# Optimization experiments

Hardware: AMD Instinct MI355X
Metric: run time of the kernel (lower is better)

The kernel has to match this reference:

```python
import jax, jax.numpy as jnp
import numpy as np


def _pn_layer(x, W):
    # x: [B, d]; W: [N, d+1, d+1]. z = [x, 1]; out[b, n] = z_b^T W_n z_b
    z = jnp.concatenate([x, jnp.ones((x.shape[0], 1), dtype=x.dtype)], axis=1)  # [B, d+1]
    zW = jnp.einsum('bi,nij->bnj', z, W)      # [B, N, d+1]
    return jnp.einsum('bnj,bj->bn', zW, z)    # [B, N]


def setup_inputs() -> dict:
    key = jax.random.key(0)
    k_x, k1, k2, k3, kw, kb = jax.random.split(key, 6)
    B, D = 2048, 256
    return {
        'x': jax.random.normal(k_x, (B, D), dtype=jnp.float32),
        'W1': jax.random.normal(k1, (256, D + 1, D + 1), dtype=jnp.float32),
        'W2': jax.random.normal(k2, (256, 257, 257), dtype=jnp.float32),
        'W3': jax.random.normal(k3, (256, 257, 257), dtype=jnp.float32),
        'w_out': jax.random.normal(kw, (1, 256), dtype=jnp.float32),
        'b_out': jax.random.normal(kb, (1,), dtype=jnp.float32),
    }


def reference(x, W1, W2, W3, w_out, b_out):
    h = _pn_layer(x, W1)   # [B, 256]
    h = _pn_layer(h, W2)   # [B, 256]
    h = _pn_layer(h, W3)   # [B, 256]
    return h @ w_out.T + b_out  # [B, 1]
```

## Files before the change

### kernel.cpp

```cpp
#include <hip/hip_runtime.h>
#include <hip/hip_bf16.h>

typedef __attribute__((ext_vector_type(8))) short short8;
typedef __attribute__((ext_vector_type(4))) float f32x4;

#define DDIM 256
#define WROW 257
#define WSTRIDE 66049
#define WT3_N 36864

__device__ __forceinline__ unsigned short f2bf(float f) {
    unsigned int u = __float_as_uint(f);
    u += 0x7fff + ((u >> 16) & 1);
    return (unsigned short)(u >> 16);
}
__device__ __forceinline__ float bf2f(unsigned short s) {
    return __uint_as_float(((unsigned int)s) << 16);
}


__global__ __launch_bounds__(256) void conv_w3_kernel(
    const float* __restrict__ Wf, unsigned short* __restrict__ Wt3,
    float* __restrict__ Vt, float* __restrict__ Dv)
{
    __shared__ float tKJ[64][65];
    __shared__ float tJK[64][65];
    const int TJ[10] = {0,1,1,2,2,2,3,3,3,3};
    const int TK[10] = {0,0,1,0,1,2,0,1,2,3};
    const int tid = threadIdx.x;
    const int n   = blockIdx.y;
    const int tj  = TJ[blockIdx.x];
    const int tk  = TK[blockIdx.x];
    const float* Wn = Wf + (size_t)n * WSTRIDE;
    if (blockIdx.x == 0) {
        int j = tid;
        Vt[n * 256 + j] = Wn[(size_t)j * WROW + 256] + Wn[65792 + j];
        if (j == 0) Dv[n] = Wn[66048];
    }
    #pragma unroll
    for (int it = 0; it < 4; ++it) {
        int idx = it * 256 + tid;
        int r   = idx >> 4;
        int c4  = (idx & 15) * 4;
        float4 vKJ = *reinterpret_cast<const float4*>(&Wn[(size_t)(tk * 64 + r) * WROW + tj * 64 + c4]);
        float4 vJK = *reinterpret_cast<const float4*>(&Wn[(size_t)(tj * 64 + r) * WROW + tk * 64 + c4]);
        tKJ[r][c4 + 0] = vKJ.x; tKJ[r][c4 + 1] = vKJ.y; tKJ[r][c4 + 2] = vKJ.z; tKJ[r][c4 + 3] = vKJ.w;
        tJK[r][c4 + 0] = vJK.x; tJK[r][c4 + 1] = vJK.y; tJK[r][c4 + 2] = vJK.z; tJK[r][c4 + 3] = vJK.w;
    }
    __syncthreads();
    const int wv = tid >> 6, lane = tid & 63;
    unsigned short* out = Wt3 + (size_t)n * WT3_N;
    int ch[8]; int nch = 0;
    #pragma unroll
    for (int jtl = 0; jtl < 2; ++jtl)
        #pragma unroll
        for (int kkl = 0; kkl < 2; ++kkl) {
            if (tk * 2 + kkl <= tj * 2 + jtl) {
                ch[nch++] = jtl * 4 + kkl * 2 + 0;
                ch[nch++] = jtl * 4 + kkl * 2 + 1;
            }
        }
    for (int c = wv; c < nch; c += 4) {
        const int jtl = ch[c] >> 2, kkl = (ch[c] >> 1) & 1, half = ch[c] & 1;
        const int jtg = tj * 2 + jtl, kkg = tk * 2 + kkl;
        const float sc = (kkg == jtg) ? 0.5f : 1.0f;
        const int jl = jtl * 32 + half * 16 + (lane & 15);
        const int k0 = kkl * 32 + (lane >> 4) * 8;
        unsigned int w[4];
        #pragma unroll
        for (int t = 0; t < 4; ++t) {
            float lo = sc * (tKJ[k0 + 2 * t][jl]     + tJK[jl][k0 + 2 * t]);
            float hi = sc * (tKJ[k0 + 2 * t + 1][jl] + tJK[jl][k0 + 2 * t + 1]);
            w[t] = (unsigned)f2bf(lo) | ((unsigned)f2bf(hi) << 16);
        }
        size_t sidx = (size_t)(jtg * (jtg + 1) / 2 + kkg) * 1024 + half * 512 + lane * 8;
        *reinterpret_cast<uint4*>(out + sidx) = make_uint4(w[0], w[1], w[2], w[3]);
    }
}

__device__ __forceinline__ void xe_gather3(const unsigned short* T, unsigned short* Xe2,
                                           int bx, int tid) {
    const int lane = tid & 63, g = tid >> 6, qw = (tid >> 4) & 3, r15 = tid & 15;
    #pragma unroll
    for (int it = 0; it < 16; ++it) {
        int c  = g * 16 + it;
        int h  = c >> 5;
        int jt = (c >> 2) & 7;
        int m  = c & 3;
        int rbase = h * 64 + m * 16 + qw * 4;
        int jA = jt * 32 + r15;
        unsigned int u0 = T[(rbase + 0) * 256 + jA];
        unsigned int u1 = T[(rbase + 1) * 256 + jA];
        unsigned int u2 = T[(rbase + 2) * 256 + jA];
        unsigned int u3 = T[(rbase + 3) * 256 + jA];
        unsigned int v0 = T[(rbase + 0) * 256 + jA + 16];
        unsigned int v1 = T[(rbase + 1) * 256 + jA + 16];
        unsigned int v2 = T[(rbase + 2) * 256 + jA + 16];
        unsigned int v3 = T[(rbase + 3) * 256 + jA + 16];
        uint4 w = make_uint4(u0 | (u1 << 16), u2 | (u3 << 16),
                             v0 | (v1 << 16), v2 | (v3 << 16));
        *reinterpret_cast<uint4*>(Xe2 + ((size_t)(bx * 2 + h) * 16384 + jt * 2048 + m * 512 + lane * 8)) = w;
    }
}

__global__ __launch_bounds__(256) void conv_x_rm_kernel(
    const float* __restrict__ X, unsigned short* __restrict__ Xbf, unsigned short* __restrict__ Xe2)
{
    __shared__ __align__(16) unsigned short T[128 * 256];
    const int tid = threadIdx.x;
    const int b0 = blockIdx.x * 128;
    const float4* Xv = reinterpret_cast<const float4*>(X + (size_t)b0 * 256);
    uint2* Xo = reinterpret_cast<uint2*>(Xbf + (size_t)b0 * 256);
    #pragma unroll
    for (int it = 0; it < 32; ++it) {
        int idx4 = it * 256 + tid;
        float4 v = Xv[idx4];
        uint2 p;
        p.x = (unsigned)f2bf(v.x) | ((unsigned)f2bf(v.y) << 16);
        p.y = (unsigned)f2bf(v.z) | ((unsigned)f2bf(v.w) << 16);
        *reinterpret_cast<uint2*>(&T[idx4 * 4]) = p;
        Xo[idx4] = p;
    }
    __syncthreads();
    xe_gather3(T, Xe2, blockIdx.x, tid);
}

__global__ __launch_bounds__(256) void conv_x_tr_kernel(
    const unsigned short* __restrict__ Hsrc, unsigned short* __restrict__ Xbf,
    unsigned short* __restrict__ Xe2)
{
    __shared__ __align__(16) unsigned short T[128 * 256];
    const int tid = threadIdx.x;
    const int b0 = blockIdx.x * 128;
    #pragma unroll
    for (int it = 0; it < 64; ++it) {
        int lin = it * 256 + tid;
        int k = lin >> 6, bp = lin & 63;
        unsigned int v = *reinterpret_cast<const unsigned int*>(Hsrc + (size_t)k * 2048 + b0 + bp * 2);
        T[(bp * 2) * 256 + k]     = (unsigned short)(v & 0xffff);
        T[(bp * 2 + 1) * 256 + k] = (unsigned short)(v >> 16);
    }
    __syncthreads();
    uint4* Xo = reinterpret_cast<uint4*>(Xbf + (size_t)b0 * 256);
    #pragma unroll
    for (int it = 0; it < 16; ++it) {
        int idx8 = it * 256 + tid;
        Xo[idx8] = *reinterpret_cast<uint4*>(&T[idx8 * 8]);
    }
    xe_gather3(T, Xe2, blockIdx.x, tid);
}

__global__ __launch_bounds__(256, 3) void pn10_kernel(
    const unsigned short* __restrict__ Xbf,
    const unsigned short* __restrict__ Xe2,
    const unsigned short* __restrict__ Wt3,
    const float* __restrict__ Vt,
    const float* __restrict__ Dv,
    unsigned short* __restrict__ Ht)
{
    __shared__ __align__(16) char Xl[32768];

    const int tid  = threadIdx.x;
    const int lane = tid & 63;
    const int wv   = tid >> 6;
    const int qw   = lane >> 4;
    const int r15  = lane & 15;

    const int fid = blockIdx.y * 32 + blockIdx.x;
    const int bt  = (fid >> 3) & 31;
    const int ng  = (fid & 7) + ((fid >> 8) << 3);
    const int n   = ng * 4 + wv;
    const int b0  = bt * 64;

    {
        const uint4* xs = reinterpret_cast<const uint4*>(Xbf + (size_t)b0 * 256);
        #pragma unroll
        for (int c = 0; c < 8; ++c) {
            int idx = c * 256 + tid;
            uint4 v = xs[idx];
            int L = idx * 16;
            int d = L ^ (((L >> 9) & 7) << 4);
            *reinterpret_cast<uint4*>(&Xl[d]) = v;
        }
    }

    const unsigned short* wp = Wt3 + (size_t)n * WT3_N + (size_t)lane * 8;
    const float* vn = Vt + n * 256;
    const unsigned short* xe = Xe2 + (size_t)bt * 16384 + (size_t)lane * 8;

    short8 bA0 = *reinterpret_cast<const short8*>(wp);
    short8 bB0 = *reinterpret_cast<const short8*>(wp + 512);
    short8 bA1 = *reinterpret_cast<const short8*>(wp + 1024);
    short8 bB1 = *reinterpret_cast<const short8*>(wp + 1024 + 512);
    short8 bA2 = *reinterpret_cast<const short8*>(wp + 2048);
    short8 bB2 = *reinterpret_cast<const short8*>(wp + 2048 + 512);
    short8 bA3 = *reinterpret_cast<const short8*>(wp + 3072);
    short8 bB3 = *reinterpret_cast<const short8*>(wp + 3072 + 512);

    short8 e0 = *reinterpret_cast<const short8*>(xe);
    short8 e1 = *reinterpret_cast<const short8*>(xe + 512);
    short8 e2 = *reinterpret_cast<const short8*>(xe + 1024);
    short8 e3 = *reinterpret_cast<const short8*>(xe + 1536);
    float vA = vn[r15], vB = vn[16 + r15];

    float ps[4][4];
    f32x4 a0[4], a1[4];
    #pragma unroll
    for (int m = 0; m < 4; ++m) {
        a0[m] = f32x4{0.f, 0.f, 0.f, 0.f};
        a1[m] = f32x4{0.f, 0.f, 0.f, 0.f};
        #pragma unroll
        for (int r = 0; r < 4; ++r) ps[m][r] = 0.f;
    }

    int jt = 0, kk = 0;
    int slab_pf = 4;

    __syncthreads();

    auto body = [&](short8& bA, short8& bB) {
        #pragma unroll
        for (int m = 0; m < 4; ++m) {
            const int row = m * 16 + r15;
            const int byte = (row * 512 + kk * 64 + qw * 16) ^ ((row & 7) << 4);
            short8 a = *reinterpret_cast<const short8*>(&Xl[byte]);
            a0[m] = __builtin_amdgcn_mfma_f32_16x16x32_bf16(a, bA, a0[m], 0, 0, 0);
            a1[m] = __builtin_amdgcn_mfma_f32_16x16x32_bf16(a, bB, a1[m], 0, 0, 0);
        }
        if (kk == jt) {
            #pragma unroll
            for (int r = 0; r < 4; ++r) {
                ps[0][r] += (a0[0][r] + vA) * bf2f((unsigned short)e0[r]) + (a1[0][r] + vB) * bf2f((unsigned short)e0[4 + r]);
                ps[1][r] += (a0[1][r] + vA) * bf2f((unsigned short)e1[r]) + (a1[1][r] + vB) * bf2f((unsigned short)e1[4 + r]);
                ps[2][r] += (a0[2][r] + vA) * bf2f((unsigned short)e2[r]) + (a1[2][r] + vB) * bf2f((unsigned short)e2[4 + r]);
                ps[3][r] += (a0[3][r] + vA) * bf2f((unsigned short)e3[r]) + (a1[3][r] + vB) * bf2f((unsigned short)e3[4 + r]);
            }
            #pragma unroll
            for (int m = 0; m < 4; ++m) {
                a0[m] = f32x4{0.f, 0.f, 0.f, 0.f};
                a1[m] = f32x4{0.f, 0.f, 0.f, 0.f};
            }
            jt += 1; kk = 0;
            const int jc = (jt < 8) ? jt : 7;
            e0 = *reinterpret_cast<const short8*>(xe + jc * 2048);
            e1 = *reinterpret_cast<const short8*>(xe + jc * 2048 + 512);
            e2 = *reinterpret_cast<const short8*>(xe + jc * 2048 + 1024);
            e3 = *reinterpret_cast<const short8*>(xe + jc * 2048 + 1536);
            vA = vn[jc * 32 + r15];
            vB = vn[jc * 32 + 16 + r15];
        } else {
            kk += 1;
        }
        const int sc = (slab_pf <= 35) ? slab_pf : 35;
        const unsigned short* pf = wp + (size_t)sc * 1024;
        bA = *reinterpret_cast<const short8*>(pf);
        bB = *reinterpret_cast<const short8*>(pf + 512);
        slab_pf += 1;
    };

    #pragma unroll 1
    for (int i = 0; i < 9; ++i) {
        body(bA0, bB0);
        body(bA1, bB1);
        body(bA2, bB2);
        body(bA3, bB3);
    }

    #pragma unroll
    for (int off = 1; off <= 8; off <<= 1)
        #pragma unroll
        for (int m = 0; m < 4; ++m)
            #pragma unroll
            for (int r = 0; r < 4; ++r) ps[m][r] += __shfl_xor(ps[m][r], off, 64);

    if (r15 == 0) {
        const float dn = Dv[n];
        #pragma unroll
        for (int m = 0; m < 4; ++m)
            #pragma unroll
            for (int r = 0; r < 4; ++r)
                Ht[(size_t)n * 2048 + b0 + m * 16 + qw * 4 + r] = f2bf(ps[m][r] + dn);
    }
}

__global__ __launch_bounds__(256) void out_tr_kernel(
    const unsigned short* __restrict__ H3, const float* __restrict__ w_out,
    const float* __restrict__ b_out, float* __restrict__ out)
{
    __shared__ float red2[256];
    const int tid = threadIdx.x;
    const int b = blockIdx.x * 128 + (tid & 127);
    const int half = tid >> 7;
    float s = 0.f;
    #pragma unroll 8
    for (int k = 0; k < 128; ++k) {
        int nn = half * 128 + k;
        s += bf2f(H3[(size_t)nn * 2048 + b]) * w_out[nn];
    }
    red2[tid] = s;
    __syncthreads();
    if (tid < 128) out[b] = red2[tid] + red2[tid + 128] + b_out[0];
}


__global__ __launch_bounds__(256, 2) void pn_layer_kernel(
    const float* __restrict__ X, const float* __restrict__ W, float* __restrict__ H)
{
    __shared__ __align__(16) char Xl[64 * 256 * 2];
    __shared__ __align__(16) char Wl[2][256 * 32 * 2];
    const int tid  = threadIdx.x;
    const int lane = tid & 63;
    const int wv   = tid >> 6;
    const int qw   = lane >> 4;
    const int r15  = lane & 15;
    const int n  = blockIdx.y;
    const int b0 = blockIdx.x * 64;
    const float* Wn = W + (size_t)n * WSTRIDE;
    {
        const float4* Xv = reinterpret_cast<const float4*>(X + (size_t)b0 * DDIM);
        #pragma unroll
        for (int it = 0; it < 16; ++it) {
            int idx4 = tid + it * 256;
            int r = idx4 >> 6, c4 = idx4 & 63;
            float4 v = Xv[r * 64 + c4];
            uint2 p;
            p.x = (unsigned)f2bf(v.x) | ((unsigned)f2bf(v.y) << 16);
            p.y = (unsigned)f2bf(v.z) | ((unsigned)f2bf(v.w) << 16);
            int byte = (r * 512 + c4 * 8) ^ ((r & 7) << 4);
            *reinterpret_cast<uint2*>(&Xl[byte]) = p;
        }
    }
    f32x4 acc[4][4];
    #pragma unroll
    for (int nf = 0; nf < 4; ++nf) {
        int j = wv * 64 + nf * 16 + r15;
        float vj = Wn[(size_t)j * WROW + 256] + Wn[65792 + j];
        #pragma unroll
        for (int m = 0; m < 4; ++m) acc[m][nf] = f32x4{vj, vj, vj, vj};
    }
    auto stageW = [&](int buf, int kk) {
        const int k0 = kk * 32;
        const int j  = tid;
        float t[32];
        #pragma unroll
        for (int k = 0; k < 32; ++k) t[k] = Wn[(size_t)(k0 + k) * WROW + j];
        char* Wb = Wl[buf];
        #pragma unroll
        for (int g = 0; g < 4; ++g) {
            unsigned int p0 = (unsigned)f2bf(t[g*8+0]) | ((unsigned)f2bf(t[g*8+1]) << 16);
            unsigned int p1 = (unsigned)f2bf(t[g*8+2]) | ((unsigned)f2bf(t[g*8+3]) << 16);
            unsigned int p2 = (unsigned)f2bf(t[g*8+4]) | ((unsigned)f2bf(t[g*8+5]) << 16);
            unsigned int p3 = (unsigned)f2bf(t[g*8+6]) | ((unsigned)f2bf(t[g*8+7]) << 16);
            int byte = (j * 64 + g * 16) ^ ((j & 7) << 4);
            *reinterpret_cast<uint4*>(&Wb[byte]) = make_uint4(p0, p1, p2, p3);
        }
    };
    auto computeK = [&](int buf, int kk) {
        char* Wb = Wl[buf];
        short8 a[4], bbf[4];
        #pragma unroll
        for (int m = 0; m < 4; ++m) {
            int row = m * 16 + r15;
            int byte = (row * 512 + kk * 64 + qw * 16) ^ ((row & 7) << 4);
            a[m] = *reinterpret_cast<short8*>(&Xl[byte]);
        }
        #pragma unroll
        for (int nf = 0; nf < 4; ++nf) {
            int j = wv * 64 + nf * 16 + r15;
            int byte = (j * 64 + qw * 16) ^ ((j & 7) << 4);
            bbf[nf] = *reinterpret_cast<short8*>(&Wb[byte]);
        }
        #pragma unroll
        for (int m = 0; m < 4; ++m)
            #pragma unroll
            for (int nf = 0; nf < 4; ++nf)
                acc[m][nf] = __builtin_amdgcn_mfma_f32_16x16x32_bf16(a[m], bbf[nf], acc[m][nf], 0, 0, 0);
    };
    stageW(0, 0);
    int cur = 0;
    #pragma unroll
    for (int kk = 0; kk < 8; ++kk) {
        __syncthreads();
        if (kk < 7) stageW(cur ^ 1, kk + 1);
        computeK(cur, kk);
        cur ^= 1;
    }
    float ps[16];
    #pragma unroll
    for (int i = 0; i < 16; ++i) ps[i] = 0.f;
    #pragma unroll
    for (int m = 0; m < 4; ++m)
        #pragma unroll
        for (int nf = 0; nf < 4; ++nf) {
            int j = wv * 64 + nf * 16 + r15;
            #pragma unroll
            for (int r = 0; r < 4; ++r) {
                int brow = m * 16 + qw * 4 + r;
                int byte = (brow * 512 + j * 2) ^ ((brow & 7) << 4);
                float xv = bf2f(*reinterpret_cast<unsigned short*>(&Xl[byte]));
                ps[m * 4 + r] += acc[m][nf][r] * xv;
            }
        }
    #pragma unroll
    for (int off = 1; off <= 8; off <<= 1)
        #pragma unroll
        for (int i = 0; i < 16; ++i) ps[i] += __shfl_xor(ps[i], off, 64);
    __syncthreads();
    float* red = reinterpret_cast<float*>(Wl);
    if (r15 == 0) {
        #pragma unroll
        for (int m = 0; m < 4; ++m)
            #pragma unroll
            for (int r = 0; r < 4; ++r)
                red[wv * 64 + m * 16 + qw * 4 + r] = ps[m * 4 + r];
    }
    __syncthreads();
    if (tid < 64) {
        float s = red[tid] + red[64 + tid] + red[128 + tid] + red[192 + tid] + Wn[66048];
        H[(size_t)(b0 + tid) * DDIM + n] = s;
    }
}

__global__ __launch_bounds__(256) void out_kernel(
    const float* __restrict__ H, const float* __restrict__ w_out,
    const float* __restrict__ b_out, float* __restrict__ out)
{
    int b = blockIdx.x * 4 + (threadIdx.x >> 6);
    int lane = threadIdx.x & 63;
    const float* h = H + (size_t)b * 256;
    float s = 0.f;
    #pragma unroll
    for (int c = 0; c < 4; ++c) s += h[lane + c * 64] * w_out[lane + c * 64];
    #pragma unroll
    for (int off = 1; off < 64; off <<= 1) s += __shfl_xor(s, off, 64);
    if (lane == 0) out[b] = s + b_out[0];
}

extern "C" void kernel_launch(void* const* d_in, const int* in_sizes, int n_in,
                              void* d_out, int out_size, void* d_ws, size_t ws_size,
                              hipStream_t stream) {
    const float* x    = (const float*)d_in[0];
    const float* W1   = (const float*)d_in[1];
    const float* W2   = (const float*)d_in[2];
    const float* W3   = (const float*)d_in[3];
    const float* wout = (const float*)d_in[4];
    const float* bout = (const float*)d_in[5];
    float* out = (float*)d_out;

    const size_t WT3_BYTES = (size_t)256 * WT3_N * 2;
    const size_t XB_BYTES  = (size_t)2048 * 256 * 2;
    const size_t XE2_BYTES = (size_t)32 * 16384 * 2;
    const size_t VT_BYTES  = 256 * 256 * 4;
    const size_t DV_BYTES  = 1024;
    const size_t HT_BYTES  = (size_t)256 * 2048 * 2;
    const size_t need = WT3_BYTES + XB_BYTES + XE2_BYTES + VT_BYTES + DV_BYTES + HT_BYTES;

    dim3 blk(256, 1, 1);

    if (ws_size >= need) {
        char* p = (char*)d_ws;
        unsigned short* Wt3 = (unsigned short*)p;              p += WT3_BYTES;
        unsigned short* Xbf = (unsigned short*)p;              p += XB_BYTES;
        unsigned short* Xe2 = (unsigned short*)p;              p += XE2_BYTES;
        float*          Vt  = (float*)p;                       p += VT_BYTES;
        float*          Dv  = (float*)p;                       p += DV_BYTES;
        unsigned short* Ht  = (unsigned short*)p;

        const float* Ws[3] = {W1, W2, W3};

        dim3 wgrid(10, 256), lgrid(32, 64), xgrid(16);
        for (int L = 0; L < 3; ++L) {
            if (L == 0) conv_x_rm_kernel<<<xgrid, blk, 0, stream>>>(x, Xbf, Xe2);
            else        conv_x_tr_kernel<<<xgrid, blk, 0, stream>>>(Ht, Xbf, Xe2);
            conv_w3_kernel<<<wgrid, blk, 0, stream>>>(Ws[L], Wt3, Vt, Dv);
            pn10_kernel<<<lgrid, blk, 0, stream>>>(Xbf, Xe2, Wt3, Vt, Dv, Ht);
        }
        out_tr_kernel<<<xgrid, blk, 0, stream>>>(Ht, wout, bout, out);
    } else {
        float* h1 = (float*)d_ws;
        float* h2 = h1 + 2048 * 256;
        dim3 grid(32, 256);
        pn_layer_kernel<<<grid, blk, 0, stream>>>(x,  W1, h1);
        pn_layer_kernel<<<grid, blk, 0, stream>>>(h1, W2, h2);
        pn_layer_kernel<<<grid, blk, 0, stream>>>(h2, W3, h1);
        out_kernel<<<512, blk, 0, stream>>>(h1, wout, bout, out);
    }
}
```

Baseline: 272.7 us.

## Process two output neurons per wave to reuse X tile LDS reads

Each wave now computes two output neurons (n0, n1) instead of one, so every LDS load of the activation fragment feeds four MFMAs instead of two. The grid is halved in y and launch bounds drop to 2 blocks per CU to make room for the doubled accumulators. Prefetch depth falls from four slabs to two double-buffered slabs, and the Xe/V loads move from prefetched registers to on-demand loads at each triangle boundary. This trades lower occupancy and less latency hiding for fewer LDS reads and less X-tile staging per neuron.

```diff
diff --git a/kernel.cpp b/kernel.cpp
--- a/kernel.cpp
+++ b/kernel.cpp
@@ -150,7 +150,7 @@
     xe_gather3(T, Xe2, blockIdx.x, tid);
 }
 
-__global__ __launch_bounds__(256, 3) void pn10_kernel(
+__global__ __launch_bounds__(256, 2) void pn13_kernel(
     const unsigned short* __restrict__ Xbf,
     const unsigned short* __restrict__ Xe2,
     const unsigned short* __restrict__ Wt3,
@@ -169,7 +169,8 @@
     const int fid = blockIdx.y * 32 + blockIdx.x;
     const int bt  = (fid >> 3) & 31;
     const int ng  = (fid & 7) + ((fid >> 8) << 3);
-    const int n   = ng * 4 + wv;
+    const int n0  = ng * 8 + wv;
+    const int n1  = n0 + 4;
     const int b0  = bt * 64;
 
     {
@@ -184,102 +185,113 @@
         }
     }
 
-    const unsigned short* wp = Wt3 + (size_t)n * WT3_N + (size_t)lane * 8;
-    const float* vn = Vt + n * 256;
+    const unsigned short* wp0 = Wt3 + (size_t)n0 * WT3_N + (size_t)lane * 8;
+    const unsigned short* wp1 = Wt3 + (size_t)n1 * WT3_N + (size_t)lane * 8;
+    const float* vn0 = Vt + n0 * 256;
+    const float* vn1 = Vt + n1 * 256;
     const unsigned short* xe = Xe2 + (size_t)bt * 16384 + (size_t)lane * 8;
 
-    short8 bA0 = *reinterpret_cast<const short8*>(wp);
-    short8 bB0 = *reinterpret_cast<const short8*>(wp + 512);
-    short8 bA1 = *reinterpret_cast<const short8*>(wp + 1024);
-    short8 bB1 = *reinterpret_cast<const short8*>(wp + 1024 + 512);
-    short8 bA2 = *reinterpret_cast<const short8*>(wp + 2048);
-    short8 bB2 = *reinterpret_cast<const short8*>(wp + 2048 + 512);
-    short8 bA3 = *reinterpret_cast<const short8*>(wp + 3072);
-    short8 bB3 = *reinterpret_cast<const short8*>(wp + 3072 + 512);
-
-    short8 e0 = *reinterpret_cast<const short8*>(xe);
-    short8 e1 = *reinterpret_cast<const short8*>(xe + 512);
-    short8 e2 = *reinterpret_cast<const short8*>(xe + 1024);
-    short8 e3 = *reinterpret_cast<const short8*>(xe + 1536);
-    float vA = vn[r15], vB = vn[16 + r15];
-
-    float ps[4][4];
-    f32x4 a0[4], a1[4];
+    short8 A0a = *reinterpret_cast<const short8*>(wp0);
+    short8 B0a = *reinterpret_cast<const short8*>(wp0 + 512);
+    short8 C0a = *reinterpret_cast<const short8*>(wp1);
+    short8 D0a = *reinterpret_cast<const short8*>(wp1 + 512);
+    short8 A0b = *reinterpret_cast<const short8*>(wp0 + 1024);
+    short8 B0b = *reinterpret_cast<const short8*>(wp0 + 1024 + 512);
+    short8 C0b = *reinterpret_cast<const short8*>(wp1 + 1024);
+    short8 D0b = *reinterpret_cast<const short8*>(wp1 + 1024 + 512);
+
+    float ps0[4][4], ps1[4][4];
+    f32x4 q0[4], q1[4], q2[4], q3[4];
     #pragma unroll
     for (int m = 0; m < 4; ++m) {
-        a0[m] = f32x4{0.f, 0.f, 0.f, 0.f};
-        a1[m] = f32x4{0.f, 0.f, 0.f, 0.f};
-        #pragma unroll
-        for (int r = 0; r < 4; ++r) ps[m][r] = 0.f;
+        q0[m] = f32x4{0.f, 0.f, 0.f, 0.f};
+        q1[m] = f32x4{0.f, 0.f, 0.f, 0.f};
+        q2[m] = f32x4{0.f, 0.f, 0.f, 0.f};
+        q3[m] = f32x4{0.f, 0.f, 0.f, 0.f};
+        #pragma unroll
+        for (int r = 0; r < 4; ++r) { ps0[m][r] = 0.f; ps1[m][r] = 0.f; }
     }
 
     int jt = 0, kk = 0;
-    int slab_pf = 4;
-
-    __syncthreads();
-
-    auto body = [&](short8& bA, short8& bB) {
+    int slab_pf = 2;
+
+    __syncthreads();
+
+    auto body = [&](short8& bA, short8& bB, short8& cA, short8& cB) {
+        const bool last = (kk == jt);
+        short8 e0, e1, e2, e3;
+        if (last) {
+            const unsigned short* ep = xe + jt * 2048;
+            e0 = *reinterpret_cast<const short8*>(ep);
+            e1 = *reinterpret_cast<const short8*>(ep + 512);
+            e2 = *reinterpret_cast<const short8*>(ep + 1024);
+            e3 = *reinterpret_cast<const short8*>(ep + 1536);
+        }
         #pragma unroll
         for (int m = 0; m < 4; ++m) {
             const int row = m * 16 + r15;
             const int byte = (row * 512 + kk * 64 + qw * 16) ^ ((row & 7) << 4);
             short8 a = *reinterpret_cast<const short8*>(&Xl[byte]);
-            a0[m] = __builtin_amdgcn_mfma_f32_16x16x32_bf16(a, bA, a0[m], 0, 0, 0);
-            a1[m] = __builtin_amdgcn_mfma_f32_16x16x32_bf16(a, bB, a1[m], 0, 0, 0);
-        }
-        if (kk == jt) {
+            q0[m] = __builtin_amdgcn_mfma_f32_16x16x32_bf16(a, bA, q0[m], 0, 0, 0);
+            q1[m] = __builtin_amdgcn_mfma_f32_16x16x32_bf16(a, bB, q1[m], 0, 0, 0);
+            q2[m] = __builtin_amdgcn_mfma_f32_16x16x32_bf16(a, cA, q2[m], 0, 0, 0);
+            q3[m] = __builtin_amdgcn_mfma_f32_16x16x32_bf16(a, cB, q3[m], 0, 0, 0);
+        }
+        if (last) {
+            const float vA0 = vn0[jt * 32 + r15], vB0 = vn0[jt * 32 + 16 + r15];
+            const float vA1 = vn1[jt * 32 + r15], vB1 = vn1[jt * 32 + 16 + r15];
+            short8 ee[4] = {e0, e1, e2, e3};
+            #pragma unroll
+            for (int m = 0; m < 4; ++m) {
+                #pragma unroll
+                for (int r = 0; r < 4; ++r) {
+                    const float exA = bf2f((unsigned short)ee[m][r]);
+                    const float exB = bf2f((unsigned short)ee[m][4 + r]);
+                    ps0[m][r] += (q0[m][r] + vA0) * exA + (q1[m][r] + vB0) * exB;
+                    ps1[m][r] += (q2[m][r] + vA1) * exA + (q3[m][r] + vB1) * exB;
+                }
+                q0[m] = f32x4{0.f, 0.f, 0.f, 0.f};
+                q1[m] = f32x4{0.f, 0.f, 0.f, 0.f};
+                q2[m] = f32x4{0.f, 0.f, 0.f, 0.f};
+                q3[m] = f32x4{0.f, 0.f, 0.f, 0.f};
+            }
+            jt += 1; kk = 0;
+        } else {
+            kk += 1;
+        }
+        const int sc = (slab_pf <= 35) ? slab_pf : 35;
+        bA = *reinterpret_cast<const short8*>(wp0 + (size_t)sc * 1024);
+        bB = *reinterpret_cast<const short8*>(wp0 + (size_t)sc * 1024 + 512);
+        cA = *reinterpret_cast<const short8*>(wp1 + (size_t)sc * 1024);
+        cB = *reinterpret_cast<const short8*>(wp1 + (size_t)sc * 1024 + 512);
+        slab_pf += 1;
+    };
+
+    #pragma unroll 1
+    for (int i = 0; i < 18; ++i) {
+        body(A0a, B0a, C0a, D0a);
+        body(A0b, B0b, C0b, D0b);
+    }
+
+    #pragma unroll
+    for (int off = 1; off <= 8; off <<= 1)
+        #pragma unroll
+        for (int m = 0; m < 4; ++m)
             #pragma unroll
             for (int r = 0; r < 4; ++r) {
-                ps[0][r] += (a0[0][r] + vA) * bf2f((unsigned short)e0[r]) + (a1[0][r] + vB) * bf2f((unsigned short)e0[4 + r]);
-                ps[1][r] += (a0[1][r] + vA) * bf2f((unsigned short)e1[r]) + (a1[1][r] + vB) * bf2f((unsigned short)e1[4 + r]);
-                ps[2][r] += (a0[2][r] + vA) * bf2f((unsigned short)e2[r]) + (a1[2][r] + vB) * bf2f((unsigned short)e2[4 + r]);
-                ps[3][r] += (a0[3][r] + vA) * bf2f((unsigned short)e3[r]) + (a1[3][r] + vB) * bf2f((unsigned short)e3[4 + r]);
+                ps0[m][r] += __shfl_xor(ps0[m][r], off, 64);
+                ps1[m][r] += __shfl_xor(ps1[m][r], off, 64);
             }
-            #pragma unroll
-            for (int m = 0; m < 4; ++m) {
-                a0[m] = f32x4{0.f, 0.f, 0.f, 0.f};
-                a1[m] = f32x4{0.f, 0.f, 0.f, 0.f};
-            }
-            jt += 1; kk = 0;
-            const int jc = (jt < 8) ? jt : 7;
-            e0 = *reinterpret_cast<const short8*>(xe + jc * 2048);
-            e1 = *reinterpret_cast<const short8*>(xe + jc * 2048 + 512);
-            e2 = *reinterpret_cast<const short8*>(xe + jc * 2048 + 1024);
-            e3 = *reinterpret_cast<const short8*>(xe + jc * 2048 + 1536);
-            vA = vn[jc * 32 + r15];
-            vB = vn[jc * 32 + 16 + r15];
-        } else {
-            kk += 1;
-        }
-        const int sc = (slab_pf <= 35) ? slab_pf : 35;
-        const unsigned short* pf = wp + (size_t)sc * 1024;
-        bA = *reinterpret_cast<const short8*>(pf);
-        bB = *reinterpret_cast<const short8*>(pf + 512);
-        slab_pf += 1;
-    };
-
-    #pragma unroll 1
-    for (int i = 0; i < 9; ++i) {
-        body(bA0, bB0);
-        body(bA1, bB1);
-        body(bA2, bB2);
-        body(bA3, bB3);
-    }
-
-    #pragma unroll
-    for (int off = 1; off <= 8; off <<= 1)
+
+    if (r15 == 0) {
+        const float dn0 = Dv[n0], dn1 = Dv[n1];
         #pragma unroll
         for (int m = 0; m < 4; ++m)
             #pragma unroll
-            for (int r = 0; r < 4; ++r) ps[m][r] += __shfl_xor(ps[m][r], off, 64);
-
-    if (r15 == 0) {
-        const float dn = Dv[n];
-        #pragma unroll
-        for (int m = 0; m < 4; ++m)
-            #pragma unroll
-            for (int r = 0; r < 4; ++r)
-                Ht[(size_t)n * 2048 + b0 + m * 16 + qw * 4 + r] = f2bf(ps[m][r] + dn);
+            for (int r = 0; r < 4; ++r) {
+                Ht[(size_t)n0 * 2048 + b0 + m * 16 + qw * 4 + r] = f2bf(ps0[m][r] + dn0);
+                Ht[(size_t)n1 * 2048 + b0 + m * 16 + qw * 4 + r] = f2bf(ps1[m][r] + dn1);
+            }
     }
 }
 
@@ -468,12 +480,12 @@
 
         const float* Ws[3] = {W1, W2, W3};
 
-        dim3 wgrid(10, 256), lgrid(32, 64), xgrid(16);
+        dim3 wgrid(10, 256), lgrid(32, 32), xgrid(16);
         for (int L = 0; L < 3; ++L) {
             if (L == 0) conv_x_rm_kernel<<<xgrid, blk, 0, stream>>>(x, Xbf, Xe2);
             else        conv_x_tr_kernel<<<xgrid, blk, 0, stream>>>(Ht, Xbf, Xe2);
             conv_w3_kernel<<<wgrid, blk, 0, stream>>>(Ws[L], Wt3, Vt, Dv);
-            pn10_kernel<<<lgrid, blk, 0, stream>>>(Xbf, Xe2, Wt3, Vt, Dv, Ht);
+            pn13_kernel<<<lgrid, blk, 0, stream>>>(Xbf, Xe2, Wt3, Vt, Dv, Ht);
         }
         out_tr_kernel<<<xgrid, blk, 0, stream>>>(Ht, wout, bout, out);
     } else {
```

Measured after the change: 260.1 us. -4.6%, faster.
